# Kernel optimization log

Measured on AMD Instinct MI355X. Metric: run time of the kernel, lower is better.

## Reference

```python
import jax, jax.numpy as jnp
import numpy as np

N_USERS, N_MOVIES, N_EDGES = 100000, 20000, 1000000
IN_UNITS, NUM_CLASSES = 128, 5


def _xavier(key, shape):
    # torch xavier_uniform_ on a Linear weight [out, in]; we store transposed [in, out]
    fan_in, fan_out = shape[0], shape[1]
    a = jnp.sqrt(6.0 / (fan_in + fan_out))
    return jax.random.uniform(key, shape, dtype=jnp.float32, minval=-a, maxval=a)


def setup_inputs() -> dict:
    key = jax.random.key(0)
    k1, k2, k3, k4, k5, k6, k7 = jax.random.split(key, 7)
    ufeat = jax.random.normal(k1, (N_USERS, IN_UNITS), dtype=jnp.float32)
    ifeat = jax.random.normal(k2, (N_MOVIES, IN_UNITS), dtype=jnp.float32)
    src_idx = jax.random.randint(k3, (N_EDGES,), 0, N_USERS, dtype=jnp.int32)
    dst_idx = jax.random.randint(k4, (N_EDGES,), 0, N_MOVIES, dtype=jnp.int32)
    W1 = _xavier(k5, (2 * IN_UNITS, IN_UNITS))   # Linear(2*in_units -> in_units)
    W2 = _xavier(k6, (IN_UNITS, IN_UNITS))       # Linear(in_units -> in_units)
    Wp = _xavier(k7, (IN_UNITS, NUM_CLASSES))    # predictor Linear(in_units -> num_classes)
    return {"ufeat": ufeat, "ifeat": ifeat, "src_idx": src_idx, "dst_idx": dst_idx,
            "W1": W1, "W2": W2, "Wp": Wp}


def reference(ufeat, ifeat, W1, W2, Wp, src_idx, dst_idx):
    # gather per-edge src/dst node features
    h_u = ufeat[src_idx]                 # [E, D]
    h_v = ifeat[dst_idx]                 # [E, D]
    h = jnp.concatenate([h_u, h_v], axis=1)          # [E, 2D]
    h = jax.nn.gelu(h @ W1, approximate=False)        # [E, D] (torch GELU default = exact erf)
    h = h @ W2                                        # [E, D]
    score = h @ Wp                                    # [E, C]
    return jnp.squeeze(score)
```

## Files before the change

### kernel.cpp

```cpp
#include <hip/hip_runtime.h>
#include <hip/hip_bf16.h>

#define D 128

typedef short bf16x8 __attribute__((ext_vector_type(8)));
typedef float f32x4 __attribute__((ext_vector_type(4)));

__device__ __forceinline__ unsigned short f2bf(float x) {
    __hip_bfloat16 h = __float2bfloat16(x);
    return *reinterpret_cast<unsigned short*>(&h);
}
__device__ __forceinline__ float bf2f(unsigned int lo16bits) {
    return __uint_as_float(lo16bits << 16);
}

__device__ __forceinline__ float gelu_tanh(float z) {
    float z2 = z * z;
    float xe = z * fmaf(0.1029466f, z2, 2.3022646f);
    float q  = __builtin_amdgcn_exp2f(xe);
    float r  = __builtin_amdgcn_rcpf(1.0f + q);
    return fmaf(-z, r, z);
}

__device__ __forceinline__ float gelu_erf(float z) {
    float y = fabsf(z) * 0.70710678118654752f;
    float t = __builtin_amdgcn_rcpf(1.0f + 0.3275911f * y);
    float poly = ((((1.061405429f * t - 1.453152027f) * t + 1.421413741f) * t
                   - 0.284496736f) * t + 0.254829592f) * t;
    float e = __expf(-y * y);
    float erfv = 1.0f - poly * e;
    erfv = copysignf(erfv, z);
    return 0.5f * z * (1.0f + erfv);
}

__device__ __forceinline__ void node_body(const float* __restrict__ feat,
                                          const float* __restrict__ W1,
                                          int base_k, int Nn, int blk,
                                          unsigned short* __restrict__ outbf) {
    __shared__ unsigned short sA[64 * 136];
    __shared__ unsigned short sB[128 * 136];
    const int t = threadIdx.x;
    const int r0 = blk * 64;

    #pragma unroll
    for (int i = 0; i < 8; ++i) {
        int f = (i * 256 + t) * 4;
        int row = f >> 7, col = f & 127;
        float4 v = make_float4(0.f, 0.f, 0.f, 0.f);
        if (r0 + row < Nn) v = *reinterpret_cast<const float4*>(&feat[(size_t)(r0 + row) * D + col]);
        unsigned short* p = &sA[row * 136 + col];
        p[0] = f2bf(v.x); p[1] = f2bf(v.y); p[2] = f2bf(v.z); p[3] = f2bf(v.w);
    }
    #pragma unroll
    for (int i = 0; i < 16; ++i) {
        int f = (i * 256 + t) * 4;
        int k = f >> 7, j = f & 127;
        float4 v = *reinterpret_cast<const float4*>(&W1[(size_t)(base_k + k) * D + j]);
        sB[(j + 0) * 136 + k] = f2bf(v.x);
        sB[(j + 1) * 136 + k] = f2bf(v.y);
        sB[(j + 2) * 136 + k] = f2bf(v.z);
        sB[(j + 3) * 136 + k] = f2bf(v.w);
    }
    __syncthreads();

    const int wid = t >> 6, l = t & 63;
    const int m16 = l & 15, g4 = l >> 4;
    f32x4 acc[8];
    #pragma unroll
    for (int n = 0; n < 8; ++n) acc[n] = (f32x4){0.f, 0.f, 0.f, 0.f};

    #pragma unroll
    for (int kk = 0; kk < 4; ++kk) {
        int k0 = kk * 32 + g4 * 8;
        bf16x8 a = *reinterpret_cast<const bf16x8*>(&sA[(wid * 16 + m16) * 136 + k0]);
        #pragma unroll
        for (int n = 0; n < 8; ++n) {
            bf16x8 b = *reinterpret_cast<const bf16x8*>(&sB[(n * 16 + m16) * 136 + k0]);
            acc[n] = __builtin_amdgcn_mfma_f32_16x16x32_bf16(a, b, acc[n], 0, 0, 0);
        }
    }
    #pragma unroll
    for (int n = 0; n < 8; ++n) {
        #pragma unroll
        for (int r = 0; r < 4; ++r) {
            int row = r0 + wid * 16 + g4 * 4 + r;
            if (row < Nn) outbf[(size_t)row * D + n * 16 + m16] = f2bf(acc[n][r]);
        }
    }
}

__global__ __launch_bounds__(256) void prep_kernel(const float* __restrict__ uf,
                                                   const float* __restrict__ vf,
                                                   const float* __restrict__ W1,
                                                   const float* __restrict__ W2,
                                                   const float* __restrict__ Wp,
                                                   int NU, int NM, int nbU, int nbM,
                                                   unsigned short* __restrict__ Abf,
                                                   unsigned short* __restrict__ Bbf,
                                                   unsigned short* __restrict__ Wcbf) {
    int b = blockIdx.x;
    if (b < nbU) {
        node_body(uf, W1, 0, NU, b, Abf);
    } else if (b < nbU + nbM) {
        node_body(vf, W1, D, NM, b - nbU, Bbf);
    } else {
        int t = threadIdx.x;
        #pragma unroll
        for (int i = 0; i < 8; ++i) {
            int idx = i * 256 + t;
            int col = idx >> 7, k = idx & 127;
            float acc = 0.f;
            if (col < 5) {
                #pragma unroll 8
                for (int j = 0; j < D; ++j) acc += W2[k * D + j] * Wp[j * 5 + col];
            }
            Wcbf[col * D + k] = f2bf(acc);
        }
    }
}

__global__ __launch_bounds__(256) void edge_kernel(const unsigned short* __restrict__ A,
                                                   const unsigned short* __restrict__ B,
                                                   const int* __restrict__ src,
                                                   const int* __restrict__ dst,
                                                   const unsigned short* __restrict__ Wcbf,
                                                   float* __restrict__ out, int E) {
    const int l    = threadIdx.x & 63;
    const int er   = l & 15;
    const int quad = l >> 4;
    const int wid  = blockIdx.x * 4 + (threadIdx.x >> 6);
    const int nw   = gridDim.x * 4;

    bf16x8 wfrag[4];
    #pragma unroll
    for (int kk = 0; kk < 4; ++kk)
        wfrag[kk] = *reinterpret_cast<const bf16x8*>(&Wcbf[er * D + kk * 32 + quad * 8]);

    const int Q = (E + 15) >> 4;
    if (wid >= Q) return;

    int q0 = wid;
    int s = src[q0 * 16 + er];
    int d = dst[q0 * 16 + er];

    for (int q = q0; q < Q; q += nw) {
        int qn = q + nw;
        int qc = qn < Q ? qn : q;
        int sn = src[qc * 16 + er];
        int dn = dst[qc * 16 + er];

        const unsigned short* ap = A + ((size_t)s << 7) + quad * 8;
        const unsigned short* bp = B + ((size_t)d << 7) + quad * 8;
        uint4 av[4], bv[4];
        #pragma unroll
        for (int kk = 0; kk < 4; ++kk) {
            av[kk] = *reinterpret_cast<const uint4*>(ap + kk * 32);
            bv[kk] = *reinterpret_cast<const uint4*>(bp + kk * 32);
        }

        f32x4 acc = (f32x4){0.f, 0.f, 0.f, 0.f};
        #pragma unroll
        for (int kk = 0; kk < 4; ++kk) {
            unsigned int aw[4] = {av[kk].x, av[kk].y, av[kk].z, av[kk].w};
            unsigned int bw[4] = {bv[kk].x, bv[kk].y, bv[kk].z, bv[kk].w};
            union { bf16x8 v; unsigned short u[8]; } frag;
            #pragma unroll
            for (int p = 0; p < 4; ++p) {
                float z0 = __uint_as_float(aw[p] << 16) + __uint_as_float(bw[p] << 16);
                float z1 = __uint_as_float(aw[p] & 0xffff0000u) + __uint_as_float(bw[p] & 0xffff0000u);
                frag.u[2 * p]     = f2bf(gelu_tanh(z0));
                frag.u[2 * p + 1] = f2bf(gelu_tanh(z1));
            }
            acc = __builtin_amdgcn_mfma_f32_16x16x32_bf16(frag.v, wfrag[kk], acc, 0, 0, 0);
        }

        int e0 = q << 4;
        #pragma unroll
        for (int r = 0; r < 4; ++r) {
            int e = e0 + quad * 4 + r;
            if (er < 5 && e < E) out[(size_t)e * 5 + er] = acc[r];
        }
        s = sn; d = dn;
    }
}

__global__ __launch_bounds__(256) void fused_fallback(const float* __restrict__ uf,
                                                      const float* __restrict__ vf,
                                                      const int* __restrict__ src,
                                                      const int* __restrict__ dst,
                                                      const float* __restrict__ W1,
                                                      const float* __restrict__ W2,
                                                      const float* __restrict__ Wp,
                                                      float* __restrict__ out, int E) {
    __shared__ unsigned short sW[256 * 128];
    __shared__ float sWc[5 * 128];
    __shared__ float sH[4][256];
    const int t = threadIdx.x;
    #pragma unroll
    for (int i = 0; i < 32; ++i) {
        int f = (i * 256 + t) * 4;
        float4 v = *reinterpret_cast<const float4*>(&W1[f]);
        sW[f + 0] = f2bf(v.x); sW[f + 1] = f2bf(v.y);
        sW[f + 2] = f2bf(v.z); sW[f + 3] = f2bf(v.w);
    }
    for (int idx = t; idx < 640; idx += 256) {
        int c = idx >> 7, k = idx & 127;
        float a = 0.f;
        for (int m = 0; m < 128; ++m) a += W2[k * 128 + m] * Wp[m * 5 + c];
        sWc[c * 128 + k] = a;
    }
    __syncthreads();
    const int wid = t >> 6, l = t & 63;
    const int nw = gridDim.x * 4;
    for (int e = blockIdx.x * 4 + wid; e < E; e += nw) {
        int s = src[e], d0 = dst[e];
        float2 hu = *reinterpret_cast<const float2*>(&uf[(size_t)s * 128 + 2 * l]);
        float2 hv = *reinterpret_cast<const float2*>(&vf[(size_t)d0 * 128 + 2 * l]);
        sH[wid][2 * l] = hu.x; sH[wid][2 * l + 1] = hu.y;
        sH[wid][128 + 2 * l] = hv.x; sH[wid][128 + 2 * l + 1] = hv.y;
        __builtin_amdgcn_wave_barrier();
        float z0 = 0.f, z1 = 0.f;
        for (int k = 0; k < 256; ++k) {
            float h = sH[wid][k];
            z0 += h * bf2f(sW[k * 128 + l]);
            z1 += h * bf2f(sW[k * 128 + l + 64]);
        }
        float g0 = gelu_erf(z0), g1 = gelu_erf(z1);
        float acc[5];
        #pragma unroll
        for (int c = 0; c < 5; ++c)
            acc[c] = g0 * sWc[c * 128 + l] + g1 * sWc[c * 128 + l + 64];
        #pragma unroll
        for (int c = 0; c < 5; ++c) {
            float v = acc[c];
            v += __shfl_xor(v, 1);  v += __shfl_xor(v, 2);
            v += __shfl_xor(v, 4);  v += __shfl_xor(v, 8);
            v += __shfl_xor(v, 16); v += __shfl_xor(v, 32);
            acc[c] = v;
        }
        float v = acc[0];
        if (l == 1) v = acc[1];
        if (l == 2) v = acc[2];
        if (l == 3) v = acc[3];
        if (l == 4) v = acc[4];
        if (l < 5) out[(size_t)e * 5 + l] = v;
        __builtin_amdgcn_wave_barrier();
    }
}

extern "C" void kernel_launch(void* const* d_in, const int* in_sizes, int n_in,
                              void* d_out, int out_size, void* d_ws, size_t ws_size,
                              hipStream_t stream) {
    const float* ufeat = (const float*)d_in[0];
    const float* ifeat = (const float*)d_in[1];
    const int*   src   = (const int*)d_in[2];
    const int*   dst   = (const int*)d_in[3];
    const float* W1    = (const float*)d_in[4];
    const float* W2    = (const float*)d_in[5];
    const float* Wp    = (const float*)d_in[6];
    float* out = (float*)d_out;

    const int NU = in_sizes[0] / D;
    const int NM = in_sizes[1] / D;
    const int E  = in_sizes[2];

    size_t off_A = 4096;
    size_t szA = (size_t)NU * D * 2;
    size_t off_B = off_A + ((szA + 255) / 256) * 256;
    size_t need = off_B + (size_t)NM * D * 2;

    if (ws_size >= need) {
        unsigned short* Wcbf = (unsigned short*)d_ws;
        unsigned short* Abf  = (unsigned short*)((char*)d_ws + off_A);
        unsigned short* Bbf  = (unsigned short*)((char*)d_ws + off_B);
        int nbU = (NU + 63) / 64, nbM = (NM + 63) / 64;
        prep_kernel<<<dim3(nbU + nbM + 1), dim3(256), 0, stream>>>(
            ufeat, ifeat, W1, W2, Wp, NU, NM, nbU, nbM, Abf, Bbf, Wcbf);
        edge_kernel<<<dim3(2048), dim3(256), 0, stream>>>(Abf, Bbf, src, dst, Wcbf, out, E);
    } else {
        fused_fallback<<<dim3(4096), dim3(256), 0, stream>>>(ufeat, ifeat, src, dst,
                                                             W1, W2, Wp, out, E);
    }
}
```

Baseline: 115.2 us.

## Process two edge tiles per wave iteration and load node features directly in prep

Each wave in the edge kernel now handles 32 edges per iteration as two 16-edge MFMA tiles, issuing eight gathered row loads before computing, to get more memory-level parallelism. The GELU is rewritten on float2 vectors to allow packed math, and launch bounds now request 4 blocks per SM. The node prep kernel drops the shared-memory staging of feature rows and reads them from global memory straight into MFMA fragments. These changes raise register pressure, which may limit occupancy or cause spills.

```diff
diff --git a/kernel.cpp b/kernel.cpp
--- a/kernel.cpp
+++ b/kernel.cpp
@@ -5,21 +5,28 @@
 
 typedef short bf16x8 __attribute__((ext_vector_type(8)));
 typedef float f32x4 __attribute__((ext_vector_type(4)));
+typedef float f32x2 __attribute__((ext_vector_type(2)));
 
 __device__ __forceinline__ unsigned short f2bf(float x) {
     __hip_bfloat16 h = __float2bfloat16(x);
     return *reinterpret_cast<unsigned short*>(&h);
 }
-__device__ __forceinline__ float bf2f(unsigned int lo16bits) {
-    return __uint_as_float(lo16bits << 16);
-}
-
-__device__ __forceinline__ float gelu_tanh(float z) {
-    float z2 = z * z;
-    float xe = z * fmaf(0.1029466f, z2, 2.3022646f);
-    float q  = __builtin_amdgcn_exp2f(xe);
-    float r  = __builtin_amdgcn_rcpf(1.0f + q);
-    return fmaf(-z, r, z);
+__device__ __forceinline__ float bflo(unsigned int w) { return __uint_as_float(w << 16); }
+__device__ __forceinline__ float bfhi(unsigned int w) { return __uint_as_float(w & 0xffff0000u); }
+
+__device__ __forceinline__ f32x2 gelu2(f32x2 z) {
+    f32x2 z2 = z * z;
+    f32x2 c1 = {0.1029466f, 0.1029466f};
+    f32x2 c0 = {2.3022646f, 2.3022646f};
+    f32x2 xe = z * __builtin_elementwise_fma(z2, c1, c0);
+    f32x2 q;
+    q.x = __builtin_amdgcn_exp2f(xe.x);
+    q.y = __builtin_amdgcn_exp2f(xe.y);
+    f32x2 d = q + 1.0f;
+    f32x2 r;
+    r.x = __builtin_amdgcn_rcpf(d.x);
+    r.y = __builtin_amdgcn_rcpf(d.y);
+    return __builtin_elementwise_fma(-z, r, z);
 }
 
 __device__ __forceinline__ float gelu_erf(float z) {
@@ -37,20 +44,10 @@
                                           const float* __restrict__ W1,
                                           int base_k, int Nn, int blk,
                                           unsigned short* __restrict__ outbf) {
-    __shared__ unsigned short sA[64 * 136];
     __shared__ unsigned short sB[128 * 136];
     const int t = threadIdx.x;
     const int r0 = blk * 64;
 
-    #pragma unroll
-    for (int i = 0; i < 8; ++i) {
-        int f = (i * 256 + t) * 4;
-        int row = f >> 7, col = f & 127;
-        float4 v = make_float4(0.f, 0.f, 0.f, 0.f);
-        if (r0 + row < Nn) v = *reinterpret_cast<const float4*>(&feat[(size_t)(r0 + row) * D + col]);
-        unsigned short* p = &sA[row * 136 + col];
-        p[0] = f2bf(v.x); p[1] = f2bf(v.y); p[2] = f2bf(v.z); p[3] = f2bf(v.w);
-    }
     #pragma unroll
     for (int i = 0; i < 16; ++i) {
         int f = (i * 256 + t) * 4;
@@ -65,6 +62,10 @@
 
     const int wid = t >> 6, l = t & 63;
     const int m16 = l & 15, g4 = l >> 4;
+    const int arow = r0 + wid * 16 + m16;
+    const bool rok = arow < Nn;
+    const float* rp = feat + (size_t)(rok ? arow : 0) * D;
+
     f32x4 acc[8];
     #pragma unroll
     for (int n = 0; n < 8; ++n) acc[n] = (f32x4){0.f, 0.f, 0.f, 0.f};
@@ -72,11 +73,18 @@
     #pragma unroll
     for (int kk = 0; kk < 4; ++kk) {
         int k0 = kk * 32 + g4 * 8;
-        bf16x8 a = *reinterpret_cast<const bf16x8*>(&sA[(wid * 16 + m16) * 136 + k0]);
+        float4 f0 = make_float4(0.f, 0.f, 0.f, 0.f), f1 = f0;
+        if (rok) {
+            f0 = *reinterpret_cast<const float4*>(rp + k0);
+            f1 = *reinterpret_cast<const float4*>(rp + k0 + 4);
+        }
+        union { bf16x8 v; unsigned short u[8]; } a;
+        a.u[0] = f2bf(f0.x); a.u[1] = f2bf(f0.y); a.u[2] = f2bf(f0.z); a.u[3] = f2bf(f0.w);
+        a.u[4] = f2bf(f1.x); a.u[5] = f2bf(f1.y); a.u[6] = f2bf(f1.z); a.u[7] = f2bf(f1.w);
         #pragma unroll
         for (int n = 0; n < 8; ++n) {
             bf16x8 b = *reinterpret_cast<const bf16x8*>(&sB[(n * 16 + m16) * 136 + k0]);
-            acc[n] = __builtin_amdgcn_mfma_f32_16x16x32_bf16(a, b, acc[n], 0, 0, 0);
+            acc[n] = __builtin_amdgcn_mfma_f32_16x16x32_bf16(a.v, b, acc[n], 0, 0, 0);
         }
     }
     #pragma unroll
@@ -119,12 +127,12 @@
     }
 }
 
-__global__ __launch_bounds__(256) void edge_kernel(const unsigned short* __restrict__ A,
-                                                   const unsigned short* __restrict__ B,
-                                                   const int* __restrict__ src,
-                                                   const int* __restrict__ dst,
-                                                   const unsigned short* __restrict__ Wcbf,
-                                                   float* __restrict__ out, int E) {
+__global__ __launch_bounds__(256, 4) void edge_kernel(const unsigned short* __restrict__ A,
+                                                      const unsigned short* __restrict__ B,
+                                                      const int* __restrict__ src,
+                                                      const int* __restrict__ dst,
+                                                      const unsigned short* __restrict__ Wcbf,
+                                                      float* __restrict__ out, int E) {
     const int l    = threadIdx.x & 63;
     const int er   = l & 15;
     const int quad = l >> 4;
@@ -136,51 +144,79 @@
     for (int kk = 0; kk < 4; ++kk)
         wfrag[kk] = *reinterpret_cast<const bf16x8*>(&Wcbf[er * D + kk * 32 + quad * 8]);
 
-    const int Q = (E + 15) >> 4;
-    if (wid >= Q) return;
-
-    int q0 = wid;
-    int s = src[q0 * 16 + er];
-    int d = dst[q0 * 16 + er];
-
-    for (int q = q0; q < Q; q += nw) {
-        int qn = q + nw;
-        int qc = qn < Q ? qn : q;
-        int sn = src[qc * 16 + er];
-        int dn = dst[qc * 16 + er];
-
-        const unsigned short* ap = A + ((size_t)s << 7) + quad * 8;
-        const unsigned short* bp = B + ((size_t)d << 7) + quad * 8;
-        uint4 av[4], bv[4];
+    const int P = (E + 31) >> 5;
+    if (wid >= P) return;
+    const int Emax = E - 1;
+
+    int ia = wid * 32 + er, ib = ia + 16;
+    int sa = src[min(ia, Emax)], da = dst[min(ia, Emax)];
+    int sb = src[min(ib, Emax)], db = dst[min(ib, Emax)];
+
+    for (int p = wid; p < P; p += nw) {
+        int pn = p + nw;
+        int pc = pn < P ? pn : p;
+        int ja = pc * 32 + er, jb = ja + 16;
+        int san = src[min(ja, Emax)], dan = dst[min(ja, Emax)];
+        int sbn = src[min(jb, Emax)], dbn = dst[min(jb, Emax)];
+
+        const unsigned short* apA = A + ((size_t)sa << 7) + quad * 8;
+        const unsigned short* bpA = B + ((size_t)da << 7) + quad * 8;
+        const unsigned short* apB = A + ((size_t)sb << 7) + quad * 8;
+        const unsigned short* bpB = B + ((size_t)db << 7) + quad * 8;
+        uint4 a0[4], b0[4], a1[4], b1[4];
         #pragma unroll
         for (int kk = 0; kk < 4; ++kk) {
-            av[kk] = *reinterpret_cast<const uint4*>(ap + kk * 32);
-            bv[kk] = *reinterpret_cast<const uint4*>(bp + kk * 32);
-        }
-
-        f32x4 acc = (f32x4){0.f, 0.f, 0.f, 0.f};
+            a0[kk] = *reinterpret_cast<const uint4*>(apA + kk * 32);
+            b0[kk] = *reinterpret_cast<const uint4*>(bpA + kk * 32);
+            a1[kk] = *reinterpret_cast<const uint4*>(apB + kk * 32);
+            b1[kk] = *reinterpret_cast<const uint4*>(bpB + kk * 32);
+        }
+
+        f32x4 accA = (f32x4){0.f, 0.f, 0.f, 0.f};
+        f32x4 accB = accA;
         #pragma unroll
         for (int kk = 0; kk < 4; ++kk) {
-            unsigned int aw[4] = {av[kk].x, av[kk].y, av[kk].z, av[kk].w};
-            unsigned int bw[4] = {bv[kk].x, bv[kk].y, bv[kk].z, bv[kk].w};
+            unsigned int aw[4] = {a0[kk].x, a0[kk].y, a0[kk].z, a0[kk].w};
+            unsigned int bw[4] = {b0[kk].x, b0[kk].y, b0[kk].z, b0[kk].w};
             union { bf16x8 v; unsigned short u[8]; } frag;
             #pragma unroll
-            for (int p = 0; p < 4; ++p) {
-                float z0 = __uint_as_float(aw[p] << 16) + __uint_as_float(bw[p] << 16);
-                float z1 = __uint_as_float(aw[p] & 0xffff0000u) + __uint_as_float(bw[p] & 0xffff0000u);
-                frag.u[2 * p]     = f2bf(gelu_tanh(z0));
-                frag.u[2 * p + 1] = f2bf(gelu_tanh(z1));
+            for (int pp = 0; pp < 4; ++pp) {
+                f32x2 za = {bflo(aw[pp]), bfhi(aw[pp])};
+                f32x2 zb = {bflo(bw[pp]), bfhi(bw[pp])};
+                f32x2 g = gelu2(za + zb);
+                frag.u[2 * pp]     = f2bf(g.x);
+                frag.u[2 * pp + 1] = f2bf(g.y);
             }
-            acc = __builtin_amdgcn_mfma_f32_16x16x32_bf16(frag.v, wfrag[kk], acc, 0, 0, 0);
-        }
-
-        int e0 = q << 4;
+            accA = __builtin_amdgcn_mfma_f32_16x16x32_bf16(frag.v, wfrag[kk], accA, 0, 0, 0);
+        }
+        #pragma unroll
+        for (int kk = 0; kk < 4; ++kk) {
+            unsigned int aw[4] = {a1[kk].x, a1[kk].y, a1[kk].z, a1[kk].w};
+            unsigned int bw[4] = {b1[kk].x, b1[kk].y, b1[kk].z, b1[kk].w};
+            union { bf16x8 v; unsigned short u[8]; } frag;
+            #pragma unroll
+            for (int pp = 0; pp < 4; ++pp) {
+                f32x2 za = {bflo(aw[pp]), bfhi(aw[pp])};
+                f32x2 zb = {bflo(bw[pp]), bfhi(bw[pp])};
+                f32x2 g = gelu2(za + zb);
+                frag.u[2 * pp]     = f2bf(g.x);
+                frag.u[2 * pp + 1] = f2bf(g.y);
+            }
+            accB = __builtin_amdgcn_mfma_f32_16x16x32_bf16(frag.v, wfrag[kk], accB, 0, 0, 0);
+        }
+
+        int e0 = p << 5;
         #pragma unroll
         for (int r = 0; r < 4; ++r) {
-            int e = e0 + quad * 4 + r;
-            if (er < 5 && e < E) out[(size_t)e * 5 + er] = acc[r];
-        }
-        s = sn; d = dn;
+            int eA = e0 + quad * 4 + r;
+            if (er < 5 && eA < E) out[(size_t)eA * 5 + er] = accA[r];
+        }
+        #pragma unroll
+        for (int r = 0; r < 4; ++r) {
+            int eB = e0 + 16 + quad * 4 + r;
+            if (er < 5 && eB < E) out[(size_t)eB * 5 + er] = accB[r];
+        }
+        sa = san; da = dan; sb = sbn; db = dbn;
     }
 }
 
@@ -222,8 +258,8 @@
         float z0 = 0.f, z1 = 0.f;
         for (int k = 0; k < 256; ++k) {
             float h = sH[wid][k];
-            z0 += h * bf2f(sW[k * 128 + l]);
-            z1 += h * bf2f(sW[k * 128 + l + 64]);
+            z0 += h * __uint_as_float((unsigned int)sW[k * 128 + l] << 16);
+            z1 += h * __uint_as_float((unsigned int)sW[k * 128 + l + 64] << 16);
         }
         float g0 = gelu_erf(z0), g1 = gelu_erf(z1);
         float acc[5];
@@ -276,7 +312,9 @@
         int nbU = (NU + 63) / 64, nbM = (NM + 63) / 64;
         prep_kernel<<<dim3(nbU + nbM + 1), dim3(256), 0, stream>>>(
             ufeat, ifeat, W1, W2, Wp, NU, NM, nbU, nbM, Abf, Bbf, Wcbf);
-        edge_kernel<<<dim3(2048), dim3(256), 0, stream>>>(Abf, Bbf, src, dst, Wcbf, out, E);
+        int P = (E + 31) >> 5;
+        int blocks = (P + 3) / 4; if (blocks > 2048) blocks = 2048;
+        edge_kernel<<<dim3(blocks), dim3(256), 0, stream>>>(Abf, Bbf, src, dst, Wcbf, out, E);
     } else {
         fused_fallback<<<dim3(4096), dim3(256), 0, stream>>>(ufeat, ifeat, src, dst,
                                                              W1, W2, Wp, out, E);
```

New measurement: 113.9 us. About the same (-1.1%).
